# Kernel optimization log

Hardware: AMD Instinct MI355X
Metric: run time of the kernel (lower is better)

Reference implementation:

```python
import jax, jax.numpy as jnp
import numpy as np

Q_MIN = 0.1            # q_min
S_B = 1.0              # s_B
BSE = 1e-3             # beta_scaling_epsilon
W_OBJ = 0.0            # weighted_obj_coordinates
EPS_LSE = 1e-3         # eps inside _beta_loss


def arctanhsq(x):
    return jnp.arctanh(x) ** 2


def select_with_default(M, x, default):
    # M: (K, W) int64 with -1 padding; x: (N, F)  ->  (K, W, F)
    g = x[jnp.maximum(M, 0)]
    return jnp.where((M >= 0)[..., None], g, default)


def scatter_to_N(x_km, M, N):
    # faithful to _scatter_to_N_indices: x[M_valid] = values, zeros elsewhere
    idx = M.reshape(-1)
    val = x_km.reshape(-1)
    safe = jnp.where(idx >= 0, idx, N)  # padded entries -> out-of-bounds -> dropped
    return jnp.zeros((N,), x_km.dtype).at[safe].set(val, mode='drop')


def setup_inputs() -> dict:
    rng = np.random.default_rng(0)
    B, Nper, Kper, C = 4, 20000, 50, 8
    N, K = B * Nper, B * Kper
    counts = rng.integers(200, 301, size=(B, Kper))  # points per object
    asso = np.full(N, -1, dtype=np.int64)            # -1 = noise
    for b in range(B):
        perm = rng.permutation(Nper) + b * Nper
        off = 0
        for j in range(Kper):
            c = int(counts[b, j])
            asso[perm[off:off + c]] = b * Kper + j
            off += c
    Mmax = int(counts.max())
    M = np.full((K, Mmax), -1, dtype=np.int64)
    for k in range(K):
        idx = np.where(asso == k)[0]
        M[k, :len(idx)] = idx
    Wn = Nper - int(counts.min())
    Mnot = np.full((K, Wn), -1, dtype=np.int64)
    for k in range(K):
        b = k // Kper
        ev = np.arange(b * Nper, (b + 1) * Nper)
        other = ev[asso[ev] != k]
        Mnot[k, :len(other)] = other
    k1, k2 = jax.random.split(jax.random.key(0))
    beta = jax.random.uniform(k1, (N, 1), jnp.float32, 1e-4, 1.0 - 1e-4)
    coords = jax.random.normal(k2, (N, C), dtype=jnp.float32)
    row_indices = np.repeat(np.arange(B), Nper).astype(np.int64)  # batch idx / point
    lengths = np.full(B, Nper, dtype=np.int64)                    # row_split lengths
    k_per_obj = np.full(K, Kper, dtype=np.int64)                  # objects in own event
    return dict(beta=beta, coords=coords, asso_idx=jnp.asarray(asso),
                M=jnp.asarray(M), M_not=jnp.asarray(Mnot),
                k_per_obj=jnp.asarray(k_per_obj),
                row_indices=jnp.asarray(row_indices), lengths=jnp.asarray(lengths))


def reference(beta, coords, asso_idx, M, M_not, k_per_obj, row_indices, lengths):
    N, K = beta.shape[0], M.shape[0]
    K_k = k_per_obj.astype(beta.dtype)[:, None]                 # (K,1)
    beta_scale = arctanhsq(beta / (1.0 + BSE)) + Q_MIN          # (N,1)
    bs_km = select_with_default(M, beta_scale, 0.0)             # (K,Mw,1)
    beta_km = select_with_default(M, beta, 0.0)
    mask_km = select_with_default(M, jnp.ones_like(beta_scale), 0.0)
    # alpha (condensation point) selection: argmax beta_scale per object
    m_idx = jnp.argmax(bs_km[:, :, 0], axis=1)
    alpha = M[jnp.arange(K), m_idx]                             # (K,)
    coords_km = select_with_default(M, coords, 0.0)             # (K,Mw,C)
    x_a = (1.0 - W_OBJ) * coords[alpha] + W_OBJ * jnp.mean(coords_km, axis=1)
    coords_k = x_a[:, None, :]                                  # (K,1,C)
    bs_k = beta_scale[alpha]                                    # (K,1)
    # attractive potential
    dsq_km = jnp.sum((coords_k - coords_km) ** 2, axis=2, keepdims=True)
    V_att = mask_km * bs_k[:, :, None] * dsq_km * bs_km
    L_V_k = jnp.sum(V_att, axis=1) / (jnp.sum(mask_km, axis=1) + 1e-6)  # (K,1)
    L_V = jnp.sum(L_V_k / K_k)
    # repulsive potential over same-event non-members
    coords_kn = select_with_default(M_not, coords, 0.0)         # (K,Wn,C)
    bs_kn = select_with_default(M_not, beta_scale, 0.0)
    mask_kn = select_with_default(M_not, jnp.ones_like(beta_scale), 0.0)
    dsq_kn = jnp.sum((coords_kn - coords_k) ** 2, axis=2, keepdims=True)
    V_rep = mask_kn * bs_k[:, :, None] * jax.nn.relu(1.0 - jnp.sqrt(dsq_kn + 1e-6)) * bs_kn
    N_kn = jnp.sum(mask_kn, axis=1) + 1e-6
    L_rep_k = jnp.sum(V_rep, axis=1) / N_kn                     # (K,1)
    L_rep = jnp.sum(L_rep_k / K_k)
    # payload scaling (normalized per object)
    pl = arctanhsq(beta / (1.0 + BSE))
    pl_km = select_with_default(M, pl, 0.0)
    pl_km = pl_km / (jnp.sum(pl_km, axis=1, keepdims=True) + 1e-12)
    # scatter per-object quantities back to N points
    L_km = jnp.broadcast_to((L_V_k + L_rep_k)[:, None, :], (K, M.shape[1], 1))
    L_V_rep = scatter_to_N(L_km, M, N)                          # (N,)
    pl_scaling = scatter_to_N(pl_km, M, N)                      # (N,)
    # beta penalty (logsumexp soft-max approximation + clamp term)
    lse = jax.scipy.special.logsumexp(beta_km / EPS_LSE, axis=1)  # (K,1)
    beta_pen = (1.0 - EPS_LSE * lse) + (1.0 - jnp.clip(jnp.sum(beta_km, axis=1), 0.0, 1.0))
    L_b = jnp.sum(beta_pen / K_k)
    # noise term: mean over row splits of mean beta on noise points
    L_noise = S_B * beta[:, 0] * (asso_idx < 0)
    sums = jax.ops.segment_sum(L_noise, row_indices, num_segments=lengths.shape[0])
    L_b = L_b + jnp.mean(sums / lengths.astype(beta.dtype))
    return (L_V, L_rep, L_b, pl_scaling, L_V_rep)
```

## Files before the change

### kernel.cpp

```cpp
#include <hip/hip_runtime.h>
#include <hip/hip_bf16.h>
#include <math.h>

#define SPLIT 8
#define CL 4

constexpr float QMIN = 0.1f;
constexpr float EPS = 0.001f;
constexpr float INV_BSE = 1.0f / 1.001f;

__device__ __forceinline__ float atanhsq(float b) {
  float a = atanhf(b * INV_BSE);
  return a * a;
}

__global__ __launch_bounds__(256) void fused_cluster_rep(
    const float* __restrict__ beta, const float* __restrict__ coords,
    const int* __restrict__ asso, const int* __restrict__ M,
    int Mmax, int Nper, int Kper, int GPB,
    float* __restrict__ k_sumV, float* __restrict__ k_cnt,
    float* __restrict__ k_bsk, float* __restrict__ k_sumpl,
    float* __restrict__ k_betapen,
    float* __restrict__ rep_part, float* __restrict__ noise_part) {
  const int G = blockIdx.x / SPLIT, s = blockIdx.x % SPLIT;
  const int b = G / GPB, gi = G % GPB;
  const int c0 = b * Kper + gi * CL;
  const int ncl = min(CL, Kper - gi * CL);
  const int w = threadIdx.x >> 6, lane = threadIdx.x & 63;

  __shared__ float s_xa[CL][8];
  __shared__ float red[CL][4];
  __shared__ float redn[4];

  if (w < ncl) {
    const int k = c0 + w;
    const int* Mrow = M + (long)k * Mmax;

    float bestV = -1.f; int bestI = 0x7fffffff; float maxb = 0.f;
    for (int i = lane; i < Mmax; i += 64) {
      int idx = Mrow[i];
      if (idx >= 0) {
        float bb = beta[idx];
        float v = atanhsq(bb) + QMIN;
        if (v > bestV || (v == bestV && i < bestI)) { bestV = v; bestI = i; }
        maxb = fmaxf(maxb, bb);
      }
    }
    #pragma unroll
    for (int o = 1; o < 64; o <<= 1) {
      float v2 = __shfl_xor(bestV, o, 64);
      int   i2 = __shfl_xor(bestI, o, 64);
      float m2 = __shfl_xor(maxb, o, 64);
      if (v2 > bestV || (v2 == bestV && i2 < bestI)) { bestV = v2; bestI = i2; }
      maxb = fmaxf(maxb, m2);
    }
    int alpha = Mrow[bestI];
    const float4* ca = reinterpret_cast<const float4*>(coords) + (long)alpha * 2;
    float4 a0 = ca[0], a1 = ca[1];
    float xa[8] = {a0.x, a0.y, a0.z, a0.w, a1.x, a1.y, a1.z, a1.w};

    float sumV = 0.f, cnt = 0.f, sumpl = 0.f, sumbeta = 0.f, sumexp = 0.f;
    for (int i = lane; i < Mmax; i += 64) {
      int idx = Mrow[i];
      if (idx >= 0) {
        const float4* c4 = reinterpret_cast<const float4*>(coords) + (long)idx * 2;
        float4 p0 = c4[0], p1 = c4[1];
        float bb = beta[idx];
        float p = atanhsq(bb);
        float d0 = p0.x-xa[0], d1 = p0.y-xa[1], d2 = p0.z-xa[2], d3 = p0.w-xa[3];
        float d4 = p1.x-xa[4], d5 = p1.y-xa[5], d6 = p1.z-xa[6], d7 = p1.w-xa[7];
        float dsq = d0*d0+d1*d1+d2*d2+d3*d3+d4*d4+d5*d5+d6*d6+d7*d7;
        sumV += dsq * (p + QMIN);
        cnt  += 1.f;
        sumpl += p;
        sumbeta += bb;
        sumexp += expf((bb - maxb) * (1.f / EPS));
      }
    }
    float vals[5] = {sumV, cnt, sumpl, sumbeta, sumexp};
    #pragma unroll
    for (int j = 0; j < 5; ++j) {
      float v = vals[j];
      #pragma unroll
      for (int o = 32; o > 0; o >>= 1) v += __shfl_down(v, o, 64);
      vals[j] = v;
    }
    if (lane < 8) s_xa[w][lane] = xa[lane];
    if (lane == 0 && s == 0) {
      float cntT = vals[1];
      float npad = (float)Mmax - cntT;
      float sumexpT = vals[4] + npad * expf(-maxb * (1.f / EPS));
      float lse = maxb * (1.f / EPS) + logf(sumexpT);
      float sb = fminf(fmaxf(vals[3], 0.f), 1.f);
      k_betapen[k] = 1.f - EPS * lse + (1.f - sb);
      k_sumV[k]  = vals[0] * bestV;
      k_cnt[k]   = cntT;
      k_bsk[k]   = bestV;
      k_sumpl[k] = vals[2];
    }
  } else {
    if (lane < 8) s_xa[w][lane] = 0.f;
  }
  __syncthreads();

  float xav[CL][8];
  #pragma unroll
  for (int c = 0; c < CL; ++c)
    #pragma unroll
    for (int j = 0; j < 8; ++j) xav[c][j] = s_xa[c][j];

  const int chunk = (Nper + SPLIT - 1) / SPLIT;
  const int lo = b * Nper + s * chunk;
  const int hi = min(b * Nper + Nper, lo + chunk);
  const bool donoise = (gi == 0);

  float srep[CL] = {0.f, 0.f, 0.f, 0.f};
  float snoise = 0.f;
  for (int n = lo + threadIdx.x; n < hi; n += 256) {
    const float4* c4 = reinterpret_cast<const float4*>(coords) + (long)n * 2;
    float4 p0 = c4[0], p1 = c4[1];
    int a = asso[n];
    float bsn = -1.f;
    #pragma unroll
    for (int c = 0; c < CL; ++c) {
      float d0 = p0.x-xav[c][0], d1 = p0.y-xav[c][1], d2 = p0.z-xav[c][2], d3 = p0.w-xav[c][3];
      float d4 = p1.x-xav[c][4], d5 = p1.y-xav[c][5], d6 = p1.z-xav[c][6], d7 = p1.w-xav[c][7];
      float dsq = d0*d0+d1*d1+d2*d2+d3*d3+d4*d4+d5*d5+d6*d6+d7*d7;
      float t = dsq + 1e-6f;
      if (t < 1.f && c < ncl && a != c0 + c) {
        if (bsn < 0.f) bsn = atanhsq(beta[n]) + QMIN;
        srep[c] += (1.f - sqrtf(t)) * bsn;
      }
    }
    if (donoise && a < 0) snoise += beta[n];
  }

  #pragma unroll
  for (int c = 0; c < CL; ++c) {
    float v = srep[c];
    #pragma unroll
    for (int o = 32; o > 0; o >>= 1) v += __shfl_down(v, o, 64);
    if (lane == 0) red[c][w] = v;
  }
  #pragma unroll
  for (int o = 32; o > 0; o >>= 1) snoise += __shfl_down(snoise, o, 64);
  if (lane == 0) redn[w] = snoise;
  __syncthreads();
  if (threadIdx.x == 0) {
    for (int c = 0; c < ncl; ++c)
      rep_part[(c0 + c) * SPLIT + s] = red[c][0] + red[c][1] + red[c][2] + red[c][3];
    if (donoise) noise_part[b * SPLIT + s] = redn[0] + redn[1] + redn[2] + redn[3];
  }
}

__global__ __launch_bounds__(256) void out_kernel(
    const float* __restrict__ beta, const int* __restrict__ asso,
    const float* __restrict__ k_sumV, const float* __restrict__ k_cnt,
    const float* __restrict__ k_bsk, const float* __restrict__ k_sumpl,
    const float* __restrict__ k_betapen,
    const float* __restrict__ rep_part, const float* __restrict__ noise_part,
    const int* __restrict__ k_per_obj, const int* __restrict__ lengths,
    int K, int B, int Nper, int N, int nb, float* __restrict__ out) {
  if (blockIdx.x == (unsigned)nb) {
    float lv = 0.f, lrep = 0.f, lb = 0.f;
    for (int k = threadIdx.x; k < K; k += 256) {
      float cnt = k_cnt[k];
      float sr = 0.f;
      #pragma unroll
      for (int ss = 0; ss < SPLIT; ++ss) sr += rep_part[k * SPLIT + ss];
      float LVk   = k_sumV[k] / (cnt + 1e-6f);
      float Lrepk = k_bsk[k] * sr / ((float)Nper - cnt + 1e-6f);
      float invK  = 1.f / (float)k_per_obj[k];
      lv   += LVk * invK;
      lrep += Lrepk * invK;
      lb   += k_betapen[k] * invK;
    }
    const int lane = threadIdx.x & 63, w = threadIdx.x >> 6;
    __shared__ float red[3][4];
    float vals[3] = {lv, lrep, lb};
    #pragma unroll
    for (int j = 0; j < 3; ++j) {
      float v = vals[j];
      #pragma unroll
      for (int o = 32; o > 0; o >>= 1) v += __shfl_down(v, o, 64);
      if (lane == 0) red[j][w] = v;
    }
    __syncthreads();
    if (threadIdx.x == 0) {
      float noiseterm = 0.f;
      for (int bb = 0; bb < B; ++bb) {
        float npb = 0.f;
        for (int ss = 0; ss < SPLIT; ++ss) npb += noise_part[bb * SPLIT + ss];
        noiseterm += npb / (float)lengths[bb];
      }
      noiseterm /= (float)B;
      out[0] = red[0][0] + red[0][1] + red[0][2] + red[0][3];
      out[1] = red[1][0] + red[1][1] + red[1][2] + red[1][3];
      out[2] = red[2][0] + red[2][1] + red[2][2] + red[2][3] + noiseterm;
    }
  } else {
    int n = blockIdx.x * 256 + threadIdx.x;
    if (n < N) {
      int a = asso[n];
      float op = 0.f, ol = 0.f;
      if (a >= 0) {
        float p = atanhsq(beta[n]);
        op = p / (k_sumpl[a] + 1e-12f);
        float cnt = k_cnt[a];
        float sr = 0.f;
        #pragma unroll
        for (int ss = 0; ss < SPLIT; ++ss) sr += rep_part[a * SPLIT + ss];
        ol = k_sumV[a] / (cnt + 1e-6f)
           + k_bsk[a] * sr / ((float)Nper - cnt + 1e-6f);
      }
      out[3 + n] = op;
      out[3 + N + n] = ol;
    }
  }
}

extern "C" void kernel_launch(void* const* d_in, const int* in_sizes, int n_in,
                              void* d_out, int out_size, void* d_ws, size_t ws_size,
                              hipStream_t stream) {
  const float* beta      = (const float*)d_in[0];
  const float* coords    = (const float*)d_in[1];
  const int*   asso      = (const int*)d_in[2];
  const int*   M         = (const int*)d_in[3];
  const int*   k_per_obj = (const int*)d_in[5];
  const int*   lengths   = (const int*)d_in[7];

  const int N    = in_sizes[0];
  const int K    = in_sizes[5];
  const int Mmax = in_sizes[3] / K;
  const int B    = in_sizes[7];
  const int Nper = N / B;
  const int Kper = K / B;
  const int GPB  = (Kper + CL - 1) / CL;

  float* ws        = (float*)d_ws;
  float* k_sumV    = ws;
  float* k_cnt     = k_sumV + K;
  float* k_bsk     = k_cnt + K;
  float* k_sumpl   = k_bsk + K;
  float* k_betapen = k_sumpl + K;
  float* rep_part  = k_betapen + K;
  float* noise_part= rep_part + K * SPLIT;

  float* out = (float*)d_out;

  const int grid1 = B * GPB * SPLIT;
  fused_cluster_rep<<<grid1, 256, 0, stream>>>(
      beta, coords, asso, M, Mmax, Nper, Kper, GPB,
      k_sumV, k_cnt, k_bsk, k_sumpl, k_betapen, rep_part, noise_part);

  const int nb = (N + 255) / 256;
  out_kernel<<<nb + 1, 256, 0, stream>>>(
      beta, asso, k_sumV, k_cnt, k_bsk, k_sumpl, k_betapen,
      rep_part, noise_part, k_per_obj, lengths, K, B, Nper, N, nb, out);
}
```

Baseline: 26.14 us.

## Split fused kernel into per-object member pass and point-parallel repulsion pass

The fused kernel is replaced by two kernels. The first computes per-object statistics with one 256-thread block per object. The second makes each point loop over all objects in its event against condensation coordinates staged in shared memory, and accumulates repulsion with shared then global atomics. Before, each block read every point of an event slice for only four objects, which re-read coords many times and parallelised poorly. The change adds a third kernel launch and atomic contention on shared accumulators, and relies on Kper fitting in KPMAX.

```diff
diff --git a/kernel.cpp b/kernel.cpp
--- a/kernel.cpp
+++ b/kernel.cpp
@@ -1,9 +1,7 @@
 #include <hip/hip_runtime.h>
-#include <hip/hip_bf16.h>
 #include <math.h>
 
-#define SPLIT 8
-#define CL 4
+#define KPMAX 64
 
 constexpr float QMIN = 0.1f;
 constexpr float EPS = 0.001f;
@@ -14,162 +12,166 @@
   return a * a;
 }
 
-__global__ __launch_bounds__(256) void fused_cluster_rep(
+__global__ __launch_bounds__(256) void member_kernel(
     const float* __restrict__ beta, const float* __restrict__ coords,
-    const int* __restrict__ asso, const int* __restrict__ M,
-    int Mmax, int Nper, int Kper, int GPB,
+    const int* __restrict__ M, int Mmax, int B,
     float* __restrict__ k_sumV, float* __restrict__ k_cnt,
     float* __restrict__ k_bsk, float* __restrict__ k_sumpl,
-    float* __restrict__ k_betapen,
-    float* __restrict__ rep_part, float* __restrict__ noise_part) {
-  const int G = blockIdx.x / SPLIT, s = blockIdx.x % SPLIT;
-  const int b = G / GPB, gi = G % GPB;
-  const int c0 = b * Kper + gi * CL;
-  const int ncl = min(CL, Kper - gi * CL);
-  const int w = threadIdx.x >> 6, lane = threadIdx.x & 63;
-
-  __shared__ float s_xa[CL][8];
-  __shared__ float red[CL][4];
-  __shared__ float redn[4];
-
-  if (w < ncl) {
-    const int k = c0 + w;
-    const int* Mrow = M + (long)k * Mmax;
-
-    float bestV = -1.f; int bestI = 0x7fffffff; float maxb = 0.f;
-    for (int i = lane; i < Mmax; i += 64) {
-      int idx = Mrow[i];
-      if (idx >= 0) {
-        float bb = beta[idx];
-        float v = atanhsq(bb) + QMIN;
-        if (v > bestV || (v == bestV && i < bestI)) { bestV = v; bestI = i; }
-        maxb = fmaxf(maxb, bb);
-      }
-    }
-    #pragma unroll
-    for (int o = 1; o < 64; o <<= 1) {
-      float v2 = __shfl_xor(bestV, o, 64);
-      int   i2 = __shfl_xor(bestI, o, 64);
-      float m2 = __shfl_xor(maxb, o, 64);
-      if (v2 > bestV || (v2 == bestV && i2 < bestI)) { bestV = v2; bestI = i2; }
-      maxb = fmaxf(maxb, m2);
+    float* __restrict__ k_betapen, float* __restrict__ k_xa,
+    float* __restrict__ k_rep, float* __restrict__ noise) {
+  const int k = blockIdx.x;
+  const int* Mrow = M + (long)k * Mmax;
+  const int lane = threadIdx.x & 63, w = threadIdx.x >> 6;
+
+  if (threadIdx.x == 0) { k_rep[k] = 0.f; if (k < B) noise[k] = 0.f; }
+
+  float bestV = -1.f; int bestI = 0x7fffffff; float maxb = 0.f;
+  for (int i = threadIdx.x; i < Mmax; i += 256) {
+    int idx = Mrow[i];
+    if (idx >= 0) {
+      float bb = beta[idx];
+      float v = atanhsq(bb) + QMIN;
+      if (v > bestV || (v == bestV && i < bestI)) { bestV = v; bestI = i; }
+      maxb = fmaxf(maxb, bb);
+    }
+  }
+  #pragma unroll
+  for (int o = 32; o > 0; o >>= 1) {
+    float v2 = __shfl_down(bestV, o, 64);
+    int   i2 = __shfl_down(bestI, o, 64);
+    float m2 = __shfl_down(maxb, o, 64);
+    if (v2 > bestV || (v2 == bestV && i2 < bestI)) { bestV = v2; bestI = i2; }
+    maxb = fmaxf(maxb, m2);
+  }
+  __shared__ float shV[4]; __shared__ int shI[4]; __shared__ float shM[4];
+  __shared__ float s_xa[8]; __shared__ float s_scal[2];
+  if (lane == 0) { shV[w] = bestV; shI[w] = bestI; shM[w] = maxb; }
+  __syncthreads();
+  if (threadIdx.x == 0) {
+    bestV = shV[0]; bestI = shI[0]; maxb = shM[0];
+    for (int ww = 1; ww < 4; ++ww) {
+      if (shV[ww] > bestV || (shV[ww] == bestV && shI[ww] < bestI)) { bestV = shV[ww]; bestI = shI[ww]; }
+      maxb = fmaxf(maxb, shM[ww]);
     }
     int alpha = Mrow[bestI];
     const float4* ca = reinterpret_cast<const float4*>(coords) + (long)alpha * 2;
     float4 a0 = ca[0], a1 = ca[1];
-    float xa[8] = {a0.x, a0.y, a0.z, a0.w, a1.x, a1.y, a1.z, a1.w};
-
-    float sumV = 0.f, cnt = 0.f, sumpl = 0.f, sumbeta = 0.f, sumexp = 0.f;
-    for (int i = lane; i < Mmax; i += 64) {
-      int idx = Mrow[i];
-      if (idx >= 0) {
-        const float4* c4 = reinterpret_cast<const float4*>(coords) + (long)idx * 2;
-        float4 p0 = c4[0], p1 = c4[1];
-        float bb = beta[idx];
-        float p = atanhsq(bb);
-        float d0 = p0.x-xa[0], d1 = p0.y-xa[1], d2 = p0.z-xa[2], d3 = p0.w-xa[3];
-        float d4 = p1.x-xa[4], d5 = p1.y-xa[5], d6 = p1.z-xa[6], d7 = p1.w-xa[7];
-        float dsq = d0*d0+d1*d1+d2*d2+d3*d3+d4*d4+d5*d5+d6*d6+d7*d7;
-        sumV += dsq * (p + QMIN);
-        cnt  += 1.f;
-        sumpl += p;
-        sumbeta += bb;
-        sumexp += expf((bb - maxb) * (1.f / EPS));
-      }
-    }
-    float vals[5] = {sumV, cnt, sumpl, sumbeta, sumexp};
-    #pragma unroll
-    for (int j = 0; j < 5; ++j) {
-      float v = vals[j];
-      #pragma unroll
-      for (int o = 32; o > 0; o >>= 1) v += __shfl_down(v, o, 64);
-      vals[j] = v;
-    }
-    if (lane < 8) s_xa[w][lane] = xa[lane];
-    if (lane == 0 && s == 0) {
-      float cntT = vals[1];
-      float npad = (float)Mmax - cntT;
-      float sumexpT = vals[4] + npad * expf(-maxb * (1.f / EPS));
-      float lse = maxb * (1.f / EPS) + logf(sumexpT);
-      float sb = fminf(fmaxf(vals[3], 0.f), 1.f);
-      k_betapen[k] = 1.f - EPS * lse + (1.f - sb);
-      k_sumV[k]  = vals[0] * bestV;
-      k_cnt[k]   = cntT;
-      k_bsk[k]   = bestV;
-      k_sumpl[k] = vals[2];
-    }
-  } else {
-    if (lane < 8) s_xa[w][lane] = 0.f;
-  }
-  __syncthreads();
-
-  float xav[CL][8];
-  #pragma unroll
-  for (int c = 0; c < CL; ++c)
-    #pragma unroll
-    for (int j = 0; j < 8; ++j) xav[c][j] = s_xa[c][j];
-
-  const int chunk = (Nper + SPLIT - 1) / SPLIT;
-  const int lo = b * Nper + s * chunk;
-  const int hi = min(b * Nper + Nper, lo + chunk);
-  const bool donoise = (gi == 0);
-
-  float srep[CL] = {0.f, 0.f, 0.f, 0.f};
-  float snoise = 0.f;
-  for (int n = lo + threadIdx.x; n < hi; n += 256) {
-    const float4* c4 = reinterpret_cast<const float4*>(coords) + (long)n * 2;
-    float4 p0 = c4[0], p1 = c4[1];
-    int a = asso[n];
-    float bsn = -1.f;
-    #pragma unroll
-    for (int c = 0; c < CL; ++c) {
-      float d0 = p0.x-xav[c][0], d1 = p0.y-xav[c][1], d2 = p0.z-xav[c][2], d3 = p0.w-xav[c][3];
-      float d4 = p1.x-xav[c][4], d5 = p1.y-xav[c][5], d6 = p1.z-xav[c][6], d7 = p1.w-xav[c][7];
+    s_xa[0]=a0.x; s_xa[1]=a0.y; s_xa[2]=a0.z; s_xa[3]=a0.w;
+    s_xa[4]=a1.x; s_xa[5]=a1.y; s_xa[6]=a1.z; s_xa[7]=a1.w;
+    s_scal[0] = bestV; s_scal[1] = maxb;
+  }
+  __syncthreads();
+  float xa[8];
+  #pragma unroll
+  for (int c = 0; c < 8; ++c) xa[c] = s_xa[c];
+  maxb = s_scal[1];
+
+  float sumV = 0.f, cnt = 0.f, sumpl = 0.f, sumbeta = 0.f, sumexp = 0.f;
+  for (int i = threadIdx.x; i < Mmax; i += 256) {
+    int idx = Mrow[i];
+    if (idx >= 0) {
+      const float4* c4 = reinterpret_cast<const float4*>(coords) + (long)idx * 2;
+      float4 p0 = c4[0], p1 = c4[1];
+      float bb = beta[idx];
+      float p = atanhsq(bb);
+      float d0 = p0.x-xa[0], d1 = p0.y-xa[1], d2 = p0.z-xa[2], d3 = p0.w-xa[3];
+      float d4 = p1.x-xa[4], d5 = p1.y-xa[5], d6 = p1.z-xa[6], d7 = p1.w-xa[7];
       float dsq = d0*d0+d1*d1+d2*d2+d3*d3+d4*d4+d5*d5+d6*d6+d7*d7;
-      float t = dsq + 1e-6f;
-      if (t < 1.f && c < ncl && a != c0 + c) {
-        if (bsn < 0.f) bsn = atanhsq(beta[n]) + QMIN;
-        srep[c] += (1.f - sqrtf(t)) * bsn;
-      }
-    }
-    if (donoise && a < 0) snoise += beta[n];
-  }
-
-  #pragma unroll
-  for (int c = 0; c < CL; ++c) {
-    float v = srep[c];
+      sumV   += dsq * (p + QMIN);
+      cnt    += 1.f;
+      sumpl  += p;
+      sumbeta+= bb;
+      sumexp += expf((bb - maxb) * (1.f / EPS));
+    }
+  }
+  __shared__ float red[5][4];
+  float vals[5] = {sumV, cnt, sumpl, sumbeta, sumexp};
+  #pragma unroll
+  for (int j = 0; j < 5; ++j) {
+    float v = vals[j];
     #pragma unroll
     for (int o = 32; o > 0; o >>= 1) v += __shfl_down(v, o, 64);
-    if (lane == 0) red[c][w] = v;
-  }
-  #pragma unroll
-  for (int o = 32; o > 0; o >>= 1) snoise += __shfl_down(snoise, o, 64);
-  if (lane == 0) redn[w] = snoise;
+    if (lane == 0) red[j][w] = v;
+  }
   __syncthreads();
   if (threadIdx.x == 0) {
-    for (int c = 0; c < ncl; ++c)
-      rep_part[(c0 + c) * SPLIT + s] = red[c][0] + red[c][1] + red[c][2] + red[c][3];
-    if (donoise) noise_part[b * SPLIT + s] = redn[0] + redn[1] + redn[2] + redn[3];
-  }
+    float t[5];
+    #pragma unroll
+    for (int j = 0; j < 5; ++j) t[j] = red[j][0] + red[j][1] + red[j][2] + red[j][3];
+    float bsk = s_scal[0];
+    float cntT = t[1];
+    float npad = (float)Mmax - cntT;
+    float sumexpT = t[4] + npad * expf(-maxb * (1.f / EPS));
+    float lse = maxb * (1.f / EPS) + logf(sumexpT);
+    float sb = fminf(fmaxf(t[3], 0.f), 1.f);
+    k_betapen[k] = 1.f - EPS * lse + (1.f - sb);
+    k_sumV[k]  = t[0] * bsk;
+    k_cnt[k]   = cntT;
+    k_bsk[k]   = bsk;
+    k_sumpl[k] = t[2];
+    #pragma unroll
+    for (int c = 0; c < 8; ++c) k_xa[(long)k * 8 + c] = s_xa[c];
+  }
+}
+
+__global__ __launch_bounds__(256) void rep_kernel(
+    const float* __restrict__ beta, const float* __restrict__ coords,
+    const int* __restrict__ asso, const float* __restrict__ k_xa,
+    int Nper, int Kper, int RPB,
+    float* __restrict__ k_rep, float* __restrict__ noise) {
+  const int b = blockIdx.x / RPB, r = blockIdx.x % RPB;
+  const int kg0 = b * Kper;
+  __shared__ float xs[KPMAX * 8];
+  __shared__ float lrep[KPMAX];
+  const int tid = threadIdx.x;
+  for (int i = tid; i < Kper * 8; i += 256) xs[i] = k_xa[(long)kg0 * 8 + i];
+  if (tid < Kper) lrep[tid] = 0.f;
+  __syncthreads();
+
+  int off = r * 256 + tid;
+  bool valid = off < Nper;
+  int n = b * Nper + (valid ? off : Nper - 1);
+  float bb = beta[n];
+  int a = valid ? asso[n] : -2147483647;
+  const float4* c4 = reinterpret_cast<const float4*>(coords) + (long)n * 2;
+  float4 p0 = c4[0], p1 = c4[1];
+  float bsn = valid ? (atanhsq(bb) + QMIN) : 0.f;
+
+  for (int k = 0; k < Kper; ++k) {
+    const float4* xv = reinterpret_cast<const float4*>(&xs[k * 8]);
+    float4 x0 = xv[0], x1 = xv[1];
+    float d0 = p0.x-x0.x, d1 = p0.y-x0.y, d2 = p0.z-x0.z, d3 = p0.w-x0.w;
+    float d4 = p1.x-x1.x, d5 = p1.y-x1.y, d6 = p1.z-x1.z, d7 = p1.w-x1.w;
+    float dsq = d0*d0+d1*d1+d2*d2+d3*d3+d4*d4+d5*d5+d6*d6+d7*d7;
+    float t = dsq + 1e-6f;
+    if (t < 1.f && a != kg0 + k)
+      atomicAdd(&lrep[k], (1.f - sqrtf(t)) * bsn);
+  }
+
+  float nsum = (valid && a < 0) ? bb : 0.f;
+  #pragma unroll
+  for (int o = 32; o > 0; o >>= 1) nsum += __shfl_down(nsum, o, 64);
+  if ((tid & 63) == 0 && nsum != 0.f) atomicAdd(&noise[b], nsum);
+
+  __syncthreads();
+  for (int k = tid; k < Kper; k += 256)
+    if (lrep[k] != 0.f) atomicAdd(&k_rep[kg0 + k], lrep[k]);
 }
 
 __global__ __launch_bounds__(256) void out_kernel(
     const float* __restrict__ beta, const int* __restrict__ asso,
     const float* __restrict__ k_sumV, const float* __restrict__ k_cnt,
     const float* __restrict__ k_bsk, const float* __restrict__ k_sumpl,
-    const float* __restrict__ k_betapen,
-    const float* __restrict__ rep_part, const float* __restrict__ noise_part,
+    const float* __restrict__ k_betapen, const float* __restrict__ k_rep,
+    const float* __restrict__ noise,
     const int* __restrict__ k_per_obj, const int* __restrict__ lengths,
     int K, int B, int Nper, int N, int nb, float* __restrict__ out) {
   if (blockIdx.x == (unsigned)nb) {
     float lv = 0.f, lrep = 0.f, lb = 0.f;
     for (int k = threadIdx.x; k < K; k += 256) {
       float cnt = k_cnt[k];
-      float sr = 0.f;
-      #pragma unroll
-      for (int ss = 0; ss < SPLIT; ++ss) sr += rep_part[k * SPLIT + ss];
       float LVk   = k_sumV[k] / (cnt + 1e-6f);
-      float Lrepk = k_bsk[k] * sr / ((float)Nper - cnt + 1e-6f);
+      float Lrepk = k_bsk[k] * k_rep[k] / ((float)Nper - cnt + 1e-6f);
       float invK  = 1.f / (float)k_per_obj[k];
       lv   += LVk * invK;
       lrep += Lrepk * invK;
@@ -188,11 +190,7 @@
     __syncthreads();
     if (threadIdx.x == 0) {
       float noiseterm = 0.f;
-      for (int bb = 0; bb < B; ++bb) {
-        float npb = 0.f;
-        for (int ss = 0; ss < SPLIT; ++ss) npb += noise_part[bb * SPLIT + ss];
-        noiseterm += npb / (float)lengths[bb];
-      }
+      for (int bb = 0; bb < B; ++bb) noiseterm += noise[bb] / (float)lengths[bb];
       noiseterm /= (float)B;
       out[0] = red[0][0] + red[0][1] + red[0][2] + red[0][3];
       out[1] = red[1][0] + red[1][1] + red[1][2] + red[1][3];
@@ -207,11 +205,8 @@
         float p = atanhsq(beta[n]);
         op = p / (k_sumpl[a] + 1e-12f);
         float cnt = k_cnt[a];
-        float sr = 0.f;
-        #pragma unroll
-        for (int ss = 0; ss < SPLIT; ++ss) sr += rep_part[a * SPLIT + ss];
         ol = k_sumV[a] / (cnt + 1e-6f)
-           + k_bsk[a] * sr / ((float)Nper - cnt + 1e-6f);
+           + k_bsk[a] * k_rep[a] / ((float)Nper - cnt + 1e-6f);
       }
       out[3 + n] = op;
       out[3 + N + n] = ol;
@@ -235,7 +230,7 @@
   const int B    = in_sizes[7];
   const int Nper = N / B;
   const int Kper = K / B;
-  const int GPB  = (Kper + CL - 1) / CL;
+  const int RPB  = (Nper + 255) / 256;
 
   float* ws        = (float*)d_ws;
   float* k_sumV    = ws;
@@ -243,18 +238,19 @@
   float* k_bsk     = k_cnt + K;
   float* k_sumpl   = k_bsk + K;
   float* k_betapen = k_sumpl + K;
-  float* rep_part  = k_betapen + K;
-  float* noise_part= rep_part + K * SPLIT;
+  float* k_xa      = k_betapen + K;
+  float* k_rep     = k_xa + (long)K * 8;
+  float* noise     = k_rep + K;
 
   float* out = (float*)d_out;
 
-  const int grid1 = B * GPB * SPLIT;
-  fused_cluster_rep<<<grid1, 256, 0, stream>>>(
-      beta, coords, asso, M, Mmax, Nper, Kper, GPB,
-      k_sumV, k_cnt, k_bsk, k_sumpl, k_betapen, rep_part, noise_part);
-
+  member_kernel<<<K, 256, 0, stream>>>(beta, coords, M, Mmax, B,
+                                       k_sumV, k_cnt, k_bsk, k_sumpl,
+                                       k_betapen, k_xa, k_rep, noise);
+  rep_kernel<<<B * RPB, 256, 0, stream>>>(beta, coords, asso, k_xa,
+                                          Nper, Kper, RPB, k_rep, noise);
   const int nb = (N + 255) / 256;
-  out_kernel<<<nb + 1, 256, 0, stream>>>(
-      beta, asso, k_sumV, k_cnt, k_bsk, k_sumpl, k_betapen,
-      rep_part, noise_part, k_per_obj, lengths, K, B, Nper, N, nb, out);
-}
+  out_kernel<<<nb + 1, 256, 0, stream>>>(beta, asso, k_sumV, k_cnt, k_bsk,
+                                         k_sumpl, k_betapen, k_rep, noise,
+                                         k_per_obj, lengths, K, B, Nper, N, nb, out);
+}
```

Measured after the change: 37.20 us. 1.42x slower.
